# Optimization experiments

Hardware: AMD Instinct MI355X
Metric: run time of the kernel (lower is better)

The kernel has to match this reference:

```python
import jax, jax.numpy as jnp
import numpy as np

N_NODES = 100000
N_EDGES = 50000
NNZ = 1600000
D = 128
L = 2


def setup_inputs() -> dict:
    key = jax.random.key(0)
    ks = jax.random.split(key, 8)
    x = jax.random.normal(ks[0], (N_NODES, D), dtype=jnp.float32)
    e = jax.random.normal(ks[1], (N_EDGES, D), dtype=jnp.float32)
    node_idx = jax.random.randint(ks[2], (NNZ,), 0, N_NODES)
    edge_idx = jax.random.randint(ks[3], (NNZ,), 0, N_EDGES)
    hyperedge_index = jnp.stack([node_idx, edge_idx]).astype(jnp.int64)
    # per-layer params: node linear, edge linear, bias; shared PReLU slope a (init 0.25)
    Wn = jax.random.normal(ks[4], (L, D, D), dtype=jnp.float32) / np.sqrt(D)
    We = jax.random.normal(ks[5], (L, D, D), dtype=jnp.float32) / np.sqrt(D)
    b = jnp.zeros((L, D), dtype=jnp.float32)
    a = jnp.array(0.25, dtype=jnp.float32)
    return {"x": x, "e": e, "hyperedge_index": hyperedge_index,
            "num_nodes": N_NODES, "num_edges": N_EDGES,
            "Wn": Wn, "We": We, "b": b, "a": a}


def reference(x, e, hyperedge_index, num_nodes, num_edges, Wn, We, b, a):
    node_idx = hyperedge_index[0]
    edge_idx = hyperedge_index[1]
    ones = jnp.ones(node_idx.shape, x.dtype)
    deg_e = jax.ops.segment_sum(ones, edge_idx, num_segments=num_edges)  # B (edge degree)
    deg_v = jax.ops.segment_sum(ones, node_idx, num_segments=num_nodes)  # D_v (node degree)
    inv_e = jnp.where(deg_e > 0, 1.0 / deg_e, 0.0)[:, None]
    inv_v = jnp.where(deg_v > 0, 1.0 / deg_v, 0.0)[:, None]
    num_layers = Wn.shape[0]
    for l in range(num_layers):
        x1 = x @ Wn[l]                                   # [N, D]
        # gather node feats per incidence, mean-aggregate onto hyperedges
        m = jax.ops.segment_sum(x1[node_idx], edge_idx, num_segments=num_edges) * inv_e  # [E, D]
        h = m + e @ We[l] + b[l]                          # hyperedge hidden [E, D]
        # scatter hyperedge messages back to nodes, degree-normalized
        x = jax.ops.segment_sum(h[edge_idx], node_idx, num_segments=num_nodes) * inv_v   # [N, D]
        x = jnp.where(x >= 0, x, a * x)                   # shared PReLU
    return x
```

## Files before the change

kernel.cpp:

```cpp
#include <hip/hip_runtime.h>

#define DD 128


__global__ __launch_bounds__(256) void hist_kernel(const int* __restrict__ nidx,
                                                   const int* __restrict__ eidx,
                                                   int* __restrict__ cnt_v,
                                                   int* __restrict__ cnt_e, int nnz) {
  int base = (blockIdx.x * 256 + threadIdx.x) * 4;
  if (base + 4 <= nnz) {
    int4 n4 = *reinterpret_cast<const int4*>(nidx + base);
    int4 e4 = *reinterpret_cast<const int4*>(eidx + base);
    atomicAdd(&cnt_v[n4.x], 1);
    atomicAdd(&cnt_v[n4.y], 1);
    atomicAdd(&cnt_v[n4.z], 1);
    atomicAdd(&cnt_v[n4.w], 1);
    atomicAdd(&cnt_e[e4.x], 1);
    atomicAdd(&cnt_e[e4.y], 1);
    atomicAdd(&cnt_e[e4.z], 1);
    atomicAdd(&cnt_e[e4.w], 1);
  } else {
    for (int i = base; i < nnz; ++i) {
      atomicAdd(&cnt_v[nidx[i]], 1);
      atomicAdd(&cnt_e[eidx[i]], 1);
    }
  }
}

__global__ __launch_bounds__(256) void partial_reduce(const int* __restrict__ cnt, int n,
                                                      int* __restrict__ partials) {
  __shared__ int s[256];
  int t = threadIdx.x;
  int base = blockIdx.x * 1024;
  int sum = 0;
#pragma unroll
  for (int k = 0; k < 4; ++k) {
    int i = base + t * 4 + k;
    if (i < n) sum += cnt[i];
  }
  s[t] = sum;
  __syncthreads();
  for (int o = 128; o > 0; o >>= 1) {
    if (t < o) s[t] += s[t + o];
    __syncthreads();
  }
  if (t == 0) partials[blockIdx.x] = s[0];
}

__global__ __launch_bounds__(256) void scan_partials(int* __restrict__ partials, int nparts,
                                                     int* __restrict__ rp, int n) {
  __shared__ int s[256];
  int t = threadIdx.x;
  int v = (t < nparts) ? partials[t] : 0;
  s[t] = v;
  __syncthreads();
  for (int o = 1; o < 256; o <<= 1) {
    int add = (t >= o) ? s[t - o] : 0;
    __syncthreads();
    s[t] += add;
    __syncthreads();
  }
  if (t < nparts) partials[t] = s[t] - v;
  if (t == 255) rp[n] = s[255];
}

__global__ __launch_bounds__(256) void scan_final(const int* __restrict__ cnt,
                                                  const int* __restrict__ partials, int n,
                                                  int* __restrict__ rp, int* __restrict__ cur) {
  __shared__ int s[256];
  int t = threadIdx.x;
  int base = blockIdx.x * 1024;
  int v[4];
  int sum = 0;
#pragma unroll
  for (int k = 0; k < 4; ++k) {
    int i = base + t * 4 + k;
    v[k] = (i < n) ? cnt[i] : 0;
    sum += v[k];
  }
  s[t] = sum;
  __syncthreads();
  int own = sum;
  for (int o = 1; o < 256; o <<= 1) {
    int add = (t >= o) ? s[t - o] : 0;
    __syncthreads();
    s[t] += add;
    __syncthreads();
  }
  int off = partials[blockIdx.x] + (s[t] - own);
#pragma unroll
  for (int k = 0; k < 4; ++k) {
    int i = base + t * 4 + k;
    if (i < n) {
      rp[i] = off;
      cur[i] = off;
      off += v[k];
    }
  }
}

__global__ __launch_bounds__(256) void fill_kernel(const int* __restrict__ nidx,
                                                   const int* __restrict__ eidx,
                                                   int* __restrict__ cur_v,
                                                   int* __restrict__ cur_e,
                                                   int* __restrict__ col_v,
                                                   int* __restrict__ col_e, int nnz) {
  int base = (blockIdx.x * 256 + threadIdx.x) * 4;
  if (base + 4 <= nnz) {
    int4 n4 = *reinterpret_cast<const int4*>(nidx + base);
    int4 e4 = *reinterpret_cast<const int4*>(eidx + base);
    int p;
    p = atomicAdd(&cur_e[e4.x], 1); col_e[p] = n4.x;
    p = atomicAdd(&cur_e[e4.y], 1); col_e[p] = n4.y;
    p = atomicAdd(&cur_e[e4.z], 1); col_e[p] = n4.z;
    p = atomicAdd(&cur_e[e4.w], 1); col_e[p] = n4.w;
    p = atomicAdd(&cur_v[n4.x], 1); col_v[p] = e4.x;
    p = atomicAdd(&cur_v[n4.y], 1); col_v[p] = e4.y;
    p = atomicAdd(&cur_v[n4.z], 1); col_v[p] = e4.z;
    p = atomicAdd(&cur_v[n4.w], 1); col_v[p] = e4.w;
  } else {
    for (int i = base; i < nnz; ++i) {
      int v = nidx[i], e = eidx[i];
      int p = atomicAdd(&cur_e[e], 1);
      col_e[p] = v;
      int q = atomicAdd(&cur_v[v], 1);
      col_v[q] = e;
    }
  }
}

__global__ __launch_bounds__(256) void gather_mlp(const float* __restrict__ x,
                                                  const int* __restrict__ rp,
                                                  const int* __restrict__ col,
                                                  const float* __restrict__ ein,
                                                  const float* __restrict__ Wn,
                                                  const float* __restrict__ We,
                                                  const float* __restrict__ bias,
                                                  float* __restrict__ h, int E) {
  const int ROWS = 16;
  __shared__ float sA[ROWS][DD];
  __shared__ float sE[ROWS][DD];
  int r0 = blockIdx.x * ROWS;
  int wave = threadIdx.x >> 6;
  int lane = threadIdx.x & 63;

#pragma unroll
  for (int rr = 0; rr < 4; ++rr) {
    int li = wave * 4 + rr;
    int row = r0 + li;
    float ax = 0.f, ay = 0.f;
    float2 ev = make_float2(0.f, 0.f);
    if (row < E) {
      int beg = rp[row], end = rp[row + 1];
      int j = beg;
      for (; j + 8 <= end; j += 8) {
        int c[8];
#pragma unroll
        for (int u = 0; u < 8; ++u) c[u] = col[j + u];
#pragma unroll
        for (int u = 0; u < 8; ++u) {
          float2 v = ((const float2*)(x + (size_t)c[u] * DD))[lane];
          ax += v.x;
          ay += v.y;
        }
      }
      for (; j < end; ++j) {
        float2 v = ((const float2*)(x + (size_t)col[j] * DD))[lane];
        ax += v.x;
        ay += v.y;
      }
      float inv = (end > beg) ? 1.f / (float)(end - beg) : 0.f;
      ax *= inv;
      ay *= inv;
      ev = ((const float2*)(ein + (size_t)row * DD))[lane];
    }
    ((float2*)&sA[li][0])[lane] = make_float2(ax, ay);
    ((float2*)&sE[li][0])[lane] = ev;
  }
  __syncthreads();

  int rg = threadIdx.x >> 5;
  int rA = rg * 2, rB = rA + 1;
  int c0 = (threadIdx.x & 31) * 4;
  float acc0[4], acc1[4];
#pragma unroll
  for (int cc = 0; cc < 4; ++cc) {
    float bv = bias[c0 + cc];
    acc0[cc] = bv;
    acc1[cc] = bv;
  }
  for (int k0 = 0; k0 < DD; k0 += 4) {
    float aA[4], aB[4], eA[4], eB[4];
    *(float4*)aA = *(const float4*)&sA[rA][k0];
    *(float4*)aB = *(const float4*)&sA[rB][k0];
    *(float4*)eA = *(const float4*)&sE[rA][k0];
    *(float4*)eB = *(const float4*)&sE[rB][k0];
#pragma unroll
    for (int kk = 0; kk < 4; ++kk) {
      float wn[4], we[4];
      *(float4*)wn = *(const float4*)&Wn[(size_t)(k0 + kk) * DD + c0];
      *(float4*)we = *(const float4*)&We[(size_t)(k0 + kk) * DD + c0];
#pragma unroll
      for (int cc = 0; cc < 4; ++cc) {
        acc0[cc] += aA[kk] * wn[cc] + eA[kk] * we[cc];
        acc1[cc] += aB[kk] * wn[cc] + eB[kk] * we[cc];
      }
    }
  }
  int rowA = r0 + rA, rowB = r0 + rB;
  if (rowA < E)
    *(float4*)&h[(size_t)rowA * DD + c0] = make_float4(acc0[0], acc0[1], acc0[2], acc0[3]);
  if (rowB < E)
    *(float4*)&h[(size_t)rowB * DD + c0] = make_float4(acc1[0], acc1[1], acc1[2], acc1[3]);
}

__global__ __launch_bounds__(256) void gather_prelu(const float* __restrict__ src,
                                                    const int* __restrict__ rp,
                                                    const int* __restrict__ col,
                                                    const float* __restrict__ a_ptr,
                                                    float* __restrict__ dst, int nrows) {
  int r = blockIdx.x * 4 + (threadIdx.x >> 6);
  if (r >= nrows) return;
  int lane = threadIdx.x & 63;
  int beg = rp[r], end = rp[r + 1];
  float ax = 0.f, ay = 0.f;
  int j = beg;
  for (; j + 8 <= end; j += 8) {
    int c[8];
#pragma unroll
    for (int u = 0; u < 8; ++u) c[u] = col[j + u];
#pragma unroll
    for (int u = 0; u < 8; ++u) {
      float2 v = ((const float2*)(src + (size_t)c[u] * DD))[lane];
      ax += v.x;
      ay += v.y;
    }
  }
  for (; j < end; ++j) {
    float2 v = ((const float2*)(src + (size_t)col[j] * DD))[lane];
    ax += v.x;
    ay += v.y;
  }
  float inv = (end > beg) ? 1.f / (float)(end - beg) : 0.f;
  float a = a_ptr[0];
  ax *= inv;
  ay *= inv;
  ax = ax >= 0.f ? ax : a * ax;
  ay = ay >= 0.f ? ay : a * ay;
  ((float2*)(dst + (size_t)r * DD))[lane] = make_float2(ax, ay);
}


extern "C" void kernel_launch(void* const* d_in, const int* in_sizes, int n_in,
                              void* d_out, int out_size, void* d_ws, size_t ws_size,
                              hipStream_t stream) {
  const float* x_in  = (const float*)d_in[0];
  const float* e_in  = (const float*)d_in[1];
  const int*   hidx  = (const int*)d_in[2];
  const float* Wn    = (const float*)d_in[5];
  const float* We    = (const float*)d_in[6];
  const float* bias  = (const float*)d_in[7];
  const float* a_ptr = (const float*)d_in[8];

  const int N   = in_sizes[0] / DD;
  const int E   = in_sizes[1] / DD;
  const int NNZ = in_sizes[2] / 2;
  const int L   = in_sizes[5] / (DD * DD);

  const int* node_idx = hidx;
  const int* edge_idx = hidx + NNZ;

  char* ws = (char*)d_ws;
  size_t off = 0;
  auto take = [&](size_t bytes) {
    void* p = ws + off;
    off = (off + bytes + 511) & ~(size_t)511;
    return p;
  };
  int* cnt_v  = (int*)take((size_t)N * 4);
  int* cnt_e  = (int*)take((size_t)E * 4);
  int* rp_v   = (int*)take((size_t)(N + 1) * 4);
  int* rp_e   = (int*)take((size_t)(E + 1) * 4);
  int* cur_v  = (int*)take((size_t)N * 4);
  int* cur_e  = (int*)take((size_t)E * 4);
  int* part_v = (int*)take(256 * 4);
  int* part_e = (int*)take(256 * 4);
  int* col_v  = (int*)take((size_t)NNZ * 4);
  int* col_e  = (int*)take((size_t)NNZ * 4);
  float* hbuf = (float*)take((size_t)E * DD * 4);

  float* xbuf = (float*)d_out;

  const int nparts_v = (N + 1023) / 1024;
  const int nparts_e = (E + 1023) / 1024;
  const int nnz4 = (NNZ + 3) / 4;

  hipMemsetAsync(cnt_v, 0, (size_t)N * 4, stream);
  hipMemsetAsync(cnt_e, 0, (size_t)E * 4, stream);
  hist_kernel<<<(nnz4 + 255) / 256, 256, 0, stream>>>(node_idx, edge_idx, cnt_v, cnt_e, NNZ);

  partial_reduce<<<nparts_v, 256, 0, stream>>>(cnt_v, N, part_v);
  partial_reduce<<<nparts_e, 256, 0, stream>>>(cnt_e, E, part_e);
  scan_partials<<<1, 256, 0, stream>>>(part_v, nparts_v, rp_v, N);
  scan_partials<<<1, 256, 0, stream>>>(part_e, nparts_e, rp_e, E);
  scan_final<<<nparts_v, 256, 0, stream>>>(cnt_v, part_v, N, rp_v, cur_v);
  scan_final<<<nparts_e, 256, 0, stream>>>(cnt_e, part_e, E, rp_e, cur_e);

  fill_kernel<<<(nnz4 + 255) / 256, 256, 0, stream>>>(node_idx, edge_idx, cur_v, cur_e,
                                                      col_v, col_e, NNZ);

  const float* x_src = x_in;
  for (int l = 0; l < L; ++l) {
    gather_mlp<<<(E + 15) / 16, 256, 0, stream>>>(x_src, rp_e, col_e, e_in,
                                                  Wn + (size_t)l * DD * DD,
                                                  We + (size_t)l * DD * DD,
                                                  bias + (size_t)l * DD, hbuf, E);
    gather_prelu<<<(N + 3) / 4, 256, 0, stream>>>(hbuf, rp_v, col_v, a_ptr, xbuf, N);
    x_src = xbuf;
  }
}
```

Before: 1.170 ms.

## Bucket CSR fill by key range, widen gather unroll, use 512-thread MLP blocks

The CSR fill is split into two kernels. Each block scans one chunk of incidences and handles only keys in one of 16 key-range buckets, so atomics and scattered column writes land in a narrower address window. The gather loops now issue 16 independent row loads before accumulating, which raises memory-level parallelism, and the remainder is handled in steps of 4. gather_mlp runs 512 threads per block, with each thread computing one row instead of two. Each incidence index is re-read 16 times by the bucketed fill, and the larger MLP block may lower occupancy and cuts weight reuse per thread.

```diff
diff --git a/kernel.cpp b/kernel.cpp
--- a/kernel.cpp
+++ b/kernel.cpp
@@ -1,6 +1,8 @@
 #include <hip/hip_runtime.h>
 
 #define DD 128
+#define FILL_BUCKETS 16
+#define FILL_CHUNK 16384
 
 
 __global__ __launch_bounds__(256) void hist_kernel(const int* __restrict__ nidx,
@@ -99,37 +101,35 @@
   }
 }
 
-__global__ __launch_bounds__(256) void fill_kernel(const int* __restrict__ nidx,
-                                                   const int* __restrict__ eidx,
-                                                   int* __restrict__ cur_v,
-                                                   int* __restrict__ cur_e,
-                                                   int* __restrict__ col_v,
-                                                   int* __restrict__ col_e, int nnz) {
-  int base = (blockIdx.x * 256 + threadIdx.x) * 4;
-  if (base + 4 <= nnz) {
-    int4 n4 = *reinterpret_cast<const int4*>(nidx + base);
-    int4 e4 = *reinterpret_cast<const int4*>(eidx + base);
-    int p;
-    p = atomicAdd(&cur_e[e4.x], 1); col_e[p] = n4.x;
-    p = atomicAdd(&cur_e[e4.y], 1); col_e[p] = n4.y;
-    p = atomicAdd(&cur_e[e4.z], 1); col_e[p] = n4.z;
-    p = atomicAdd(&cur_e[e4.w], 1); col_e[p] = n4.w;
-    p = atomicAdd(&cur_v[n4.x], 1); col_v[p] = e4.x;
-    p = atomicAdd(&cur_v[n4.y], 1); col_v[p] = e4.y;
-    p = atomicAdd(&cur_v[n4.z], 1); col_v[p] = e4.z;
-    p = atomicAdd(&cur_v[n4.w], 1); col_v[p] = e4.w;
-  } else {
-    for (int i = base; i < nnz; ++i) {
-      int v = nidx[i], e = eidx[i];
-      int p = atomicAdd(&cur_e[e], 1);
-      col_e[p] = v;
-      int q = atomicAdd(&cur_v[v], 1);
-      col_v[q] = e;
-    }
-  }
-}
-
-__global__ __launch_bounds__(256) void gather_mlp(const float* __restrict__ x,
+__global__ __launch_bounds__(256) void fill_bucketed(const int* __restrict__ key,
+                                                     const int* __restrict__ val,
+                                                     int* __restrict__ cur,
+                                                     int* __restrict__ colout,
+                                                     int nnz, int bsize) {
+  int bucket = blockIdx.x & (FILL_BUCKETS - 1);
+  int chunk = blockIdx.x / FILL_BUCKETS;
+  int lo = bucket * bsize;
+  int hi = lo + bsize;
+  int cbeg = chunk * FILL_CHUNK;
+  int cend = min(nnz, cbeg + FILL_CHUNK);
+  for (int i = cbeg + threadIdx.x * 4; i < cend; i += 256 * 4) {
+    if (i + 4 <= cend) {
+      int4 k4 = *reinterpret_cast<const int4*>(key + i);
+      int4 v4 = *reinterpret_cast<const int4*>(val + i);
+      if (k4.x >= lo && k4.x < hi) { int p = atomicAdd(&cur[k4.x], 1); colout[p] = v4.x; }
+      if (k4.y >= lo && k4.y < hi) { int p = atomicAdd(&cur[k4.y], 1); colout[p] = v4.y; }
+      if (k4.z >= lo && k4.z < hi) { int p = atomicAdd(&cur[k4.z], 1); colout[p] = v4.z; }
+      if (k4.w >= lo && k4.w < hi) { int p = atomicAdd(&cur[k4.w], 1); colout[p] = v4.w; }
+    } else {
+      for (int j = i; j < cend; ++j) {
+        int k = key[j];
+        if (k >= lo && k < hi) { int p = atomicAdd(&cur[k], 1); colout[p] = val[j]; }
+      }
+    }
+  }
+}
+
+__global__ __launch_bounds__(512) void gather_mlp(const float* __restrict__ x,
                                                   const int* __restrict__ rp,
                                                   const int* __restrict__ col,
                                                   const float* __restrict__ ein,
@@ -145,20 +145,33 @@
   int lane = threadIdx.x & 63;
 
 #pragma unroll
-  for (int rr = 0; rr < 4; ++rr) {
-    int li = wave * 4 + rr;
+  for (int rr = 0; rr < 2; ++rr) {
+    int li = wave * 2 + rr;
     int row = r0 + li;
     float ax = 0.f, ay = 0.f;
     float2 ev = make_float2(0.f, 0.f);
     if (row < E) {
       int beg = rp[row], end = rp[row + 1];
       int j = beg;
-      for (; j + 8 <= end; j += 8) {
-        int c[8];
-#pragma unroll
-        for (int u = 0; u < 8; ++u) c[u] = col[j + u];
-#pragma unroll
-        for (int u = 0; u < 8; ++u) {
+      for (; j + 16 <= end; j += 16) {
+        int c[16];
+#pragma unroll
+        for (int u = 0; u < 16; ++u) c[u] = col[j + u];
+        float2 v[16];
+#pragma unroll
+        for (int u = 0; u < 16; ++u) v[u] = ((const float2*)(x + (size_t)c[u] * DD))[lane];
+#pragma unroll
+        for (int u = 0; u < 16; ++u) {
+          ax += v[u].x;
+          ay += v[u].y;
+        }
+      }
+      for (; j + 4 <= end; j += 4) {
+        int c[4];
+#pragma unroll
+        for (int u = 0; u < 4; ++u) c[u] = col[j + u];
+#pragma unroll
+        for (int u = 0; u < 4; ++u) {
           float2 v = ((const float2*)(x + (size_t)c[u] * DD))[lane];
           ax += v.x;
           ay += v.y;
@@ -180,21 +193,17 @@
   __syncthreads();
 
   int rg = threadIdx.x >> 5;
-  int rA = rg * 2, rB = rA + 1;
   int c0 = (threadIdx.x & 31) * 4;
-  float acc0[4], acc1[4];
-#pragma unroll
-  for (int cc = 0; cc < 4; ++cc) {
-    float bv = bias[c0 + cc];
-    acc0[cc] = bv;
-    acc1[cc] = bv;
-  }
+  float acc[4];
+  float bv[4];
+  *(float4*)bv = *(const float4*)&bias[c0];
+#pragma unroll
+  for (int cc = 0; cc < 4; ++cc) acc[cc] = bv[cc];
+
   for (int k0 = 0; k0 < DD; k0 += 4) {
-    float aA[4], aB[4], eA[4], eB[4];
-    *(float4*)aA = *(const float4*)&sA[rA][k0];
-    *(float4*)aB = *(const float4*)&sA[rB][k0];
-    *(float4*)eA = *(const float4*)&sE[rA][k0];
-    *(float4*)eB = *(const float4*)&sE[rB][k0];
+    float aA[4], eA[4];
+    *(float4*)aA = *(const float4*)&sA[rg][k0];
+    *(float4*)eA = *(const float4*)&sE[rg][k0];
 #pragma unroll
     for (int kk = 0; kk < 4; ++kk) {
       float wn[4], we[4];
@@ -202,16 +211,13 @@
       *(float4*)we = *(const float4*)&We[(size_t)(k0 + kk) * DD + c0];
 #pragma unroll
       for (int cc = 0; cc < 4; ++cc) {
-        acc0[cc] += aA[kk] * wn[cc] + eA[kk] * we[cc];
-        acc1[cc] += aB[kk] * wn[cc] + eB[kk] * we[cc];
-      }
-    }
-  }
-  int rowA = r0 + rA, rowB = r0 + rB;
-  if (rowA < E)
-    *(float4*)&h[(size_t)rowA * DD + c0] = make_float4(acc0[0], acc0[1], acc0[2], acc0[3]);
-  if (rowB < E)
-    *(float4*)&h[(size_t)rowB * DD + c0] = make_float4(acc1[0], acc1[1], acc1[2], acc1[3]);
+        acc[cc] += aA[kk] * wn[cc] + eA[kk] * we[cc];
+      }
+    }
+  }
+  int row = r0 + rg;
+  if (row < E)
+    *(float4*)&h[(size_t)row * DD + c0] = make_float4(acc[0], acc[1], acc[2], acc[3]);
 }
 
 __global__ __launch_bounds__(256) void gather_prelu(const float* __restrict__ src,
@@ -225,12 +231,25 @@
   int beg = rp[r], end = rp[r + 1];
   float ax = 0.f, ay = 0.f;
   int j = beg;
-  for (; j + 8 <= end; j += 8) {
-    int c[8];
-#pragma unroll
-    for (int u = 0; u < 8; ++u) c[u] = col[j + u];
-#pragma unroll
-    for (int u = 0; u < 8; ++u) {
+  for (; j + 16 <= end; j += 16) {
+    int c[16];
+#pragma unroll
+    for (int u = 0; u < 16; ++u) c[u] = col[j + u];
+    float2 v[16];
+#pragma unroll
+    for (int u = 0; u < 16; ++u) v[u] = ((const float2*)(src + (size_t)c[u] * DD))[lane];
+#pragma unroll
+    for (int u = 0; u < 16; ++u) {
+      ax += v[u].x;
+      ay += v[u].y;
+    }
+  }
+  for (; j + 4 <= end; j += 4) {
+    int c[4];
+#pragma unroll
+    for (int u = 0; u < 4; ++u) c[u] = col[j + u];
+#pragma unroll
+    for (int u = 0; u < 4; ++u) {
       float2 v = ((const float2*)(src + (size_t)c[u] * DD))[lane];
       ax += v.x;
       ay += v.y;
@@ -294,6 +313,9 @@
   const int nparts_v = (N + 1023) / 1024;
   const int nparts_e = (E + 1023) / 1024;
   const int nnz4 = (NNZ + 3) / 4;
+  const int nchunks = (NNZ + FILL_CHUNK - 1) / FILL_CHUNK;
+  const int bsize_e = (E + FILL_BUCKETS - 1) / FILL_BUCKETS;
+  const int bsize_v = (N + FILL_BUCKETS - 1) / FILL_BUCKETS;
 
   hipMemsetAsync(cnt_v, 0, (size_t)N * 4, stream);
   hipMemsetAsync(cnt_e, 0, (size_t)E * 4, stream);
@@ -306,12 +328,14 @@
   scan_final<<<nparts_v, 256, 0, stream>>>(cnt_v, part_v, N, rp_v, cur_v);
   scan_final<<<nparts_e, 256, 0, stream>>>(cnt_e, part_e, E, rp_e, cur_e);
 
-  fill_kernel<<<(nnz4 + 255) / 256, 256, 0, stream>>>(node_idx, edge_idx, cur_v, cur_e,
-                                                      col_v, col_e, NNZ);
+  fill_bucketed<<<nchunks * FILL_BUCKETS, 256, 0, stream>>>(edge_idx, node_idx, cur_e,
+                                                            col_e, NNZ, bsize_e);
+  fill_bucketed<<<nchunks * FILL_BUCKETS, 256, 0, stream>>>(node_idx, edge_idx, cur_v,
+                                                            col_v, NNZ, bsize_v);
 
   const float* x_src = x_in;
   for (int l = 0; l < L; ++l) {
-    gather_mlp<<<(E + 15) / 16, 256, 0, stream>>>(x_src, rp_e, col_e, e_in,
+    gather_mlp<<<(E + 15) / 16, 512, 0, stream>>>(x_src, rp_e, col_e, e_in,
                                                   Wn + (size_t)l * DD * DD,
                                                   We + (size_t)l * DD * DD,
                                                   bias + (size_t)l * DD, hbuf, E);
```

New measurement: 1.166 ms. Within noise of the previous version (-0.3%).
